# Kernel optimization log

Hardware: AMD Instinct MI355X
Metric: run time of the kernel (lower is better)

The kernel has to match this reference:

```python
import jax, jax.numpy as jnp
import numpy as np

B, S, T = 64, 512, 32
H2 = 1024          # hidden_size * 2
ATT = 512          # attention_size


def setup_inputs() -> dict:
    key = jax.random.key(0)
    k1, k2, k3, k4, k5, k6 = jax.random.split(key, 6)
    h = jax.random.normal(k1, (B, S, H2), dtype=jnp.float32)
    h_mask = jax.random.randint(k2, (B, S), 0, 2).astype(jnp.int32)
    ht = jax.random.normal(k3, (B, T, H2), dtype=jnp.float32)
    # Linear params (xavier-ish scale)
    w1_w = jax.random.normal(k4, (ATT, 2 * H2), dtype=jnp.float32) * (1.0 / np.sqrt(2 * H2))
    w1_b = jax.random.normal(k5, (ATT,), dtype=jnp.float32) * 0.02
    u_w = jax.random.normal(k6, (1, ATT), dtype=jnp.float32) * (1.0 / np.sqrt(ATT))
    return {"h": h, "h_mask": h_mask, "ht": ht, "w1_w": w1_w, "w1_b": w1_b, "u_w": u_w}


def reference(h, h_mask, ht, w1_w, w1_b, u_w):
    # h: [B,S,2H], ht: [B,T,2H], h_mask: [B,S] (1 = valid, 0 = pad)
    valid = h_mask != 0                                  # [B,S]
    ht_mean = jnp.mean(ht, axis=1, keepdims=True)        # [B,1,2H]
    h_cat = jnp.concatenate(
        [h, jnp.broadcast_to(ht_mean, h.shape)], axis=2)  # [B,S,4H]
    h_cat = jnp.where(valid[..., None], h_cat, 0.0)
    a = jnp.tanh(jnp.einsum('bsf,af->bsa', h_cat, w1_w) + w1_b)  # [B,S,ATT]
    a = jnp.where(valid[..., None], a, 0.0)
    beta = jnp.einsum('bsa,a->bs', a, u_w[0])            # [B,S]
    beta = jnp.where(valid, beta, -1e20)
    alpha = jax.nn.softmax(beta, axis=1)                 # [B,S]
    s = jnp.einsum('bs,bsd->bd', alpha, h)               # [B,2H]
    return s
```

## Files before the change

### kernel.cpp

```cpp
#include <hip/hip_runtime.h>
#include <math.h>
#include <stdint.h>

#define Bb 64
#define Ss 512
#define Tt 32
#define H2 1024
#define FF 2048
#define ATT 512
#define MM (Bb * Ss)

#define BM 64
#define BN 512
#define BK 32

typedef short bf8 __attribute__((ext_vector_type(8)));
typedef short bf4 __attribute__((ext_vector_type(4)));
typedef float f4 __attribute__((ext_vector_type(4)));

__device__ __forceinline__ unsigned short f2bf(float f) {
    unsigned u = __float_as_uint(f);
    u = (u + 0x7fffu + ((u >> 16) & 1u)) >> 16;
    return (unsigned short)u;
}

__device__ __forceinline__ void gl_lds16(const void* g, void* l) {
    __builtin_amdgcn_global_load_lds((const __attribute__((address_space(1))) void*)g,
                                     (__attribute__((address_space(3))) void*)l, 16, 0, 0);
}

__global__ void init_kernel(float* __restrict__ out) {
    int i = blockIdx.x * 256 + threadIdx.x;
    out[i] = 0.0f;
}

__global__ void mean_kernel(const float* __restrict__ ht, float* __restrict__ ht_mean) {
    int b = blockIdx.x;
    int d4 = threadIdx.x;
    const float4* p = (const float4*)(ht + (size_t)b * Tt * H2);
    float4 acc = make_float4(0.f, 0.f, 0.f, 0.f);
    #pragma unroll 4
    for (int t = 0; t < Tt; ++t) {
        float4 v = p[(size_t)t * (H2 / 4) + d4];
        acc.x += v.x; acc.y += v.y; acc.z += v.z; acc.w += v.w;
    }
    const float inv = 1.0f / (float)Tt;
    acc.x *= inv; acc.y *= inv; acc.z *= inv; acc.w *= inv;
    ((float4*)(ht_mean + (size_t)b * H2))[d4] = acc;
}

__global__ __launch_bounds__(256) void c2_kernel2(const float* __restrict__ ht_mean,
                                                  const float* __restrict__ w1_w,
                                                  const float* __restrict__ w1_b,
                                                  float* __restrict__ c2) {
    __shared__ float hm[H2];
    int b = blockIdx.x;
    for (int i = threadIdx.x; i < H2; i += 256) hm[i] = ht_mean[(size_t)b * H2 + i];
    __syncthreads();
    int a = blockIdx.y * 64 + ((int)threadIdx.x >> 2);
    int q = (int)threadIdx.x & 3;
    const float4* w   = (const float4*)(w1_w + (size_t)a * FF + H2 + q * 256);
    const float4* hm4 = (const float4*)(hm + q * 256);
    float acc = 0.f;
    #pragma unroll 8
    for (int k = 0; k < 64; ++k) {
        float4 wv = w[k]; float4 hv = hm4[k];
        acc += wv.x * hv.x + wv.y * hv.y + wv.z * hv.z + wv.w * hv.w;
    }
    acc += __shfl_xor(acc, 1);
    acc += __shfl_xor(acc, 2);
    if (q == 0) c2[(size_t)b * ATT + a] = acc + w1_b[a];
}

__global__ void convw_kernel(const float* __restrict__ w1_w, unsigned short* __restrict__ out) {
    size_t e = ((size_t)blockIdx.x * 256 + threadIdx.x) * 8;
    int row = (int)(e >> 10);
    int c = (int)(e & 1023);
    const float* src = w1_w + (size_t)row * FF + c;
    float4 a = *(const float4*)(src);
    float4 b = *(const float4*)(src + 4);
    bf8 v = { (short)f2bf(a.x), (short)f2bf(a.y), (short)f2bf(a.z), (short)f2bf(a.w),
              (short)f2bf(b.x), (short)f2bf(b.y), (short)f2bf(b.z), (short)f2bf(b.w) };
    *(bf8*)(out + e) = v;
}

__global__ __launch_bounds__(512) void gemm_fused_kernel(
        const float* __restrict__ h, const unsigned short* __restrict__ wb,
        const float* __restrict__ c2, const float* __restrict__ u_w,
        float* __restrict__ beta) {
    __shared__ __align__(16) unsigned short As[BM][BK];
    __shared__ __align__(16) unsigned short Bs[BN][BK];
    __shared__ float red[8][64];

    const int tid = (int)threadIdx.x;
    const int m0 = blockIdx.x * BM;
    const int wid = tid >> 6, lane = tid & 63;
    const int col = lane & 15, rg = lane >> 4;

    f4 acc[4][4] = {};

    const int arow = tid >> 3;
    const int aq   = (tid & 7) * 4;
    const float* Ag = h + (size_t)(m0 + arow) * H2 + aq;
    const int brow = tid >> 2;
    const int bq   = (tid & 3) * 8;
    unsigned short* lB = &Bs[0][0] + (size_t)wid * 512;

    for (int k0 = 0; k0 < H2; k0 += BK) {
        #pragma unroll
        for (int c = 0; c < 4; ++c)
            gl_lds16(wb + (size_t)(c * 128 + brow) * H2 + k0 + bq, lB + c * 4096);
        float4 a4 = *(const float4*)(Ag + k0);
        bf4 ab = { (short)f2bf(a4.x), (short)f2bf(a4.y), (short)f2bf(a4.z), (short)f2bf(a4.w) };
        *(bf4*)&As[arow][aq] = ab;
        __syncthreads();
        bf8 av[4], bv[4];
        #pragma unroll
        for (int i = 0; i < 4; ++i) {
            av[i] = *(const bf8*)&As[i * 16 + col][rg * 8];
            bv[i] = *(const bf8*)&Bs[wid * 64 + i * 16 + col][rg * 8];
        }
        #pragma unroll
        for (int i = 0; i < 4; ++i)
            #pragma unroll
            for (int j = 0; j < 4; ++j)
                acc[i][j] = __builtin_amdgcn_mfma_f32_16x16x32_bf16(av[i], bv[j], acc[i][j], 0, 0, 0);
        __syncthreads();
    }

    const int b_idx = blockIdx.x >> 3;
    const float* c2b = c2 + (size_t)b_idx * ATT + wid * 64;
    const float* ub  = u_w + wid * 64;
    float rp[4][4] = {};
    #pragma unroll
    for (int j = 0; j < 4; ++j) {
        int n = j * 16 + col;
        float cv = c2b[n];
        float uv = ub[n];
        #pragma unroll
        for (int i = 0; i < 4; ++i)
            #pragma unroll
            for (int r = 0; r < 4; ++r)
                rp[i][r] += tanhf(acc[i][j][r] + cv) * uv;
    }
    #pragma unroll
    for (int i = 0; i < 4; ++i)
        #pragma unroll
        for (int r = 0; r < 4; ++r) {
            float v = rp[i][r];
            v += __shfl_xor(v, 1);
            v += __shfl_xor(v, 2);
            v += __shfl_xor(v, 4);
            v += __shfl_xor(v, 8);
            if (col == 0) red[wid][i * 16 + rg * 4 + r] = v;
        }
    __syncthreads();
    if (tid < 64) {
        float s = 0.f;
        #pragma unroll
        for (int w = 0; w < 8; ++w) s += red[w][tid];
        beta[(size_t)m0 + tid] = s;
    }
}

__global__ void softmax_kernel(const float* __restrict__ beta, const int* __restrict__ h_mask,
                               float* __restrict__ alpha) {
    __shared__ float red[16];
    int b = blockIdx.x;
    int s = (int)threadIdx.x;
    float v = (h_mask[(size_t)b * Ss + s] != 0) ? beta[(size_t)b * Ss + s] : -1e20f;
    float m = v;
    #pragma unroll
    for (int off = 32; off >= 1; off >>= 1) m = fmaxf(m, __shfl_xor(m, off, 64));
    int wave = s >> 6;
    if ((s & 63) == 0) red[wave] = m;
    __syncthreads();
    float mx = red[0];
    #pragma unroll
    for (int w = 1; w < 8; ++w) mx = fmaxf(mx, red[w]);
    float e = expf(v - mx);
    float sum = e;
    #pragma unroll
    for (int off = 32; off >= 1; off >>= 1) sum += __shfl_xor(sum, off, 64);
    __syncthreads();
    if ((s & 63) == 0) red[8 + wave] = sum;
    __syncthreads();
    float tot = 0.f;
    #pragma unroll
    for (int w = 0; w < 8; ++w) tot += red[8 + w];
    alpha[(size_t)b * Ss + s] = e / tot;
}

__global__ void wsum_kernel(const float* __restrict__ h, const float* __restrict__ alpha,
                            float* __restrict__ out) {
    int b = blockIdx.x;
    int d = blockIdx.y * 256 + (int)threadIdx.x;
    int s0 = blockIdx.z * 128;
    const float* hp = h + (size_t)b * Ss * H2 + (size_t)s0 * H2 + d;
    const float* ap = alpha + (size_t)b * Ss + s0;
    float acc = 0.f;
    #pragma unroll 4
    for (int s = 0; s < 128; ++s) acc = fmaf(ap[s], hp[(size_t)s * H2], acc);
    atomicAdd(&out[(size_t)b * H2 + d], acc);
}

extern "C" void kernel_launch(void* const* d_in, const int* in_sizes, int n_in,
                              void* d_out, int out_size, void* d_ws, size_t ws_size,
                              hipStream_t stream) {
    const float* h      = (const float*)d_in[0];
    const int*   h_mask = (const int*)d_in[1];
    const float* ht     = (const float*)d_in[2];
    const float* w1_w   = (const float*)d_in[3];
    const float* w1_b   = (const float*)d_in[4];
    const float* u_w    = (const float*)d_in[5];
    float* out = (float*)d_out;

    float* ws      = (float*)d_ws;
    float* ht_mean = ws;
    float* c2      = ws + 65536;
    float* beta    = ws + 98304;
    float* alpha   = ws + 131072;
    unsigned short* w1a_bf = (unsigned short*)(ws + 164864);

    hipLaunchKernelGGL(init_kernel, dim3(Bb * H2 / 256), dim3(256), 0, stream, out);
    hipLaunchKernelGGL(mean_kernel, dim3(Bb), dim3(256), 0, stream, ht, ht_mean);
    hipLaunchKernelGGL(c2_kernel2, dim3(Bb, 8), dim3(256), 0, stream, ht_mean, w1_w, w1_b, c2);
    hipLaunchKernelGGL(convw_kernel, dim3(256), dim3(256), 0, stream, w1_w, w1a_bf);
    hipLaunchKernelGGL(gemm_fused_kernel, dim3(MM / BM), dim3(512), 0, stream,
                       h, w1a_bf, c2, u_w, beta);
    hipLaunchKernelGGL(softmax_kernel, dim3(Bb), dim3(512), 0, stream, beta, h_mask, alpha);
    hipLaunchKernelGGL(wsum_kernel, dim3(Bb, H2 / 256, 4), dim3(256), 0, stream, h, alpha, out);
}
```

Baseline: 341.2 us.

## Double-buffer GEMM tiles with swizzled LDS layout and fast tanh

The fused GEMM now double-buffers its A and B tiles in shared memory. The next K-slice's global loads (direct-to-LDS for weights, register prefetch for activations) are issued before the MFMA work on the current slice, so there is one barrier per iteration instead of two. The LDS layout is XOR-swizzled to cut bank conflicts on the bf8 fragment reads. tanhf is replaced by an exp-based approximation, and launch bounds now request higher occupancy. The costs are double the LDS footprint, which may limit occupancy, and slightly different tanh numerics.

After: 294.4 us. -13.7%, faster.

```diff
diff --git a/kernel.cpp b/kernel.cpp
--- a/kernel.cpp
+++ b/kernel.cpp
@@ -27,6 +27,10 @@
 __device__ __forceinline__ void gl_lds16(const void* g, void* l) {
     __builtin_amdgcn_global_load_lds((const __attribute__((address_space(1))) void*)g,
                                      (__attribute__((address_space(3))) void*)l, 16, 0, 0);
+}
+
+__device__ __forceinline__ float tanh_fast(float x) {
+    return 1.0f - 2.0f / (__expf(2.0f * x) + 1.0f);
 }
 
 __global__ void init_kernel(float* __restrict__ out) {
@@ -84,48 +88,69 @@
     *(bf8*)(out + e) = v;
 }
 
-__global__ __launch_bounds__(512) void gemm_fused_kernel(
+__global__ __launch_bounds__(512, 4) void gemm_fused2_kernel(
         const float* __restrict__ h, const unsigned short* __restrict__ wb,
         const float* __restrict__ c2, const float* __restrict__ u_w,
         float* __restrict__ beta) {
-    __shared__ __align__(16) unsigned short As[BM][BK];
-    __shared__ __align__(16) unsigned short Bs[BN][BK];
+    __shared__ __align__(16) unsigned short As[2][BM * BK];
+    __shared__ __align__(16) unsigned short Bs[2][BN * BK];
     __shared__ float red[8][64];
 
     const int tid = (int)threadIdx.x;
     const int m0 = blockIdx.x * BM;
     const int wid = tid >> 6, lane = tid & 63;
     const int col = lane & 15, rg = lane >> 4;
+    const int rswz = rg ^ ((col >> 1) & 3);
 
     f4 acc[4][4] = {};
 
     const int arow = tid >> 3;
-    const int aq   = (tid & 7) * 4;
-    const float* Ag = h + (size_t)(m0 + arow) * H2 + aq;
+    const int asub = tid & 7;
+    const int a_elem = arow * BK + ((((asub >> 1) ^ ((arow >> 1) & 3)) * 8) + (asub & 1) * 4);
+    const float* Ag = h + (size_t)(m0 + arow) * H2 + asub * 4;
+
     const int brow = tid >> 2;
-    const int bq   = (tid & 3) * 8;
-    unsigned short* lB = &Bs[0][0] + (size_t)wid * 512;
-
-    for (int k0 = 0; k0 < H2; k0 += BK) {
-        #pragma unroll
-        for (int c = 0; c < 4; ++c)
-            gl_lds16(wb + (size_t)(c * 128 + brow) * H2 + k0 + bq, lB + c * 4096);
-        float4 a4 = *(const float4*)(Ag + k0);
+    const int bslot_src = (tid & 3) ^ ((tid >> 3) & 3);
+    const int ldsbase = wid * 512;
+
+    #pragma unroll
+    for (int c = 0; c < 4; ++c)
+        gl_lds16(wb + (size_t)(c * 128 + brow) * H2 + bslot_src * 8,
+                 &Bs[0][ldsbase + c * 4096]);
+    {
+        float4 a4 = *(const float4*)(Ag);
         bf4 ab = { (short)f2bf(a4.x), (short)f2bf(a4.y), (short)f2bf(a4.z), (short)f2bf(a4.w) };
-        *(bf4*)&As[arow][aq] = ab;
-        __syncthreads();
+        *(bf4*)&As[0][a_elem] = ab;
+    }
+    __syncthreads();
+
+    int cur = 0;
+    for (int t = 0; t < 32; ++t) {
+        float4 a4n;
+        if (t < 31) {
+            a4n = *(const float4*)(Ag + (t + 1) * BK);
+            #pragma unroll
+            for (int c = 0; c < 4; ++c)
+                gl_lds16(wb + (size_t)(c * 128 + brow) * H2 + (t + 1) * BK + bslot_src * 8,
+                         &Bs[cur ^ 1][ldsbase + c * 4096]);
+        }
         bf8 av[4], bv[4];
         #pragma unroll
         for (int i = 0; i < 4; ++i) {
-            av[i] = *(const bf8*)&As[i * 16 + col][rg * 8];
-            bv[i] = *(const bf8*)&Bs[wid * 64 + i * 16 + col][rg * 8];
+            av[i] = *(const bf8*)&As[cur][(i * 16 + col) * BK + rswz * 8];
+            bv[i] = *(const bf8*)&Bs[cur][(wid * 64 + i * 16 + col) * BK + rswz * 8];
         }
         #pragma unroll
         for (int i = 0; i < 4; ++i)
             #pragma unroll
             for (int j = 0; j < 4; ++j)
                 acc[i][j] = __builtin_amdgcn_mfma_f32_16x16x32_bf16(av[i], bv[j], acc[i][j], 0, 0, 0);
+        if (t < 31) {
+            bf4 ab = { (short)f2bf(a4n.x), (short)f2bf(a4n.y), (short)f2bf(a4n.z), (short)f2bf(a4n.w) };
+            *(bf4*)&As[cur ^ 1][a_elem] = ab;
+        }
         __syncthreads();
+        cur ^= 1;
     }
 
     const int b_idx = blockIdx.x >> 3;
@@ -141,7 +166,7 @@
         for (int i = 0; i < 4; ++i)
             #pragma unroll
             for (int r = 0; r < 4; ++r)
-                rp[i][r] += tanhf(acc[i][j][r] + cv) * uv;
+                rp[i][r] += tanh_fast(acc[i][j][r] + cv) * uv;
     }
     #pragma unroll
     for (int i = 0; i < 4; ++i)
@@ -226,7 +251,7 @@
     hipLaunchKernelGGL(mean_kernel, dim3(Bb), dim3(256), 0, stream, ht, ht_mean);
     hipLaunchKernelGGL(c2_kernel2, dim3(Bb, 8), dim3(256), 0, stream, ht_mean, w1_w, w1_b, c2);
     hipLaunchKernelGGL(convw_kernel, dim3(256), dim3(256), 0, stream, w1_w, w1a_bf);
-    hipLaunchKernelGGL(gemm_fused_kernel, dim3(MM / BM), dim3(512), 0, stream,
+    hipLaunchKernelGGL(gemm_fused2_kernel, dim3(MM / BM), dim3(512), 0, stream,
                        h, w1a_bf, c2, u_w, beta);
     hipLaunchKernelGGL(softmax_kernel, dim3(Bb), dim3(512), 0, stream, beta, h_mask, alpha);
     hipLaunchKernelGGL(wsum_kernel, dim3(Bb, H2 / 256, 4), dim3(256), 0, stream, h, alpha, out);
```
